# Kernel optimization log

Measured on AMD Instinct MI355X. Metric: run time of the kernel, lower is better.

Reference implementation:

```python
import jax, jax.numpy as jnp
import numpy as np

N_HEAD, D_MODEL, D_K, D_V, MAX_NEIGHBOR = 8, 512, 64, 64, 5
BS, SEQ = 2, 1024


def setup_inputs() -> dict:
    key = jax.random.key(0)
    ks = jax.random.split(key, 12)
    inp = {
        'q': jax.random.normal(ks[0], (BS, SEQ, D_MODEL), jnp.float32),
        'k': jax.random.normal(ks[1], (BS, SEQ, D_MODEL), jnp.float32),
        'v': jax.random.normal(ks[2], (BS, SEQ, D_MODEL), jnp.float32),
        'mask': jnp.ones((BS, SEQ, SEQ), jnp.int32),
        'dist': jax.random.randint(ks[3], (BS, SEQ, SEQ), 0, 10, jnp.int32),
        # weights stored as (in, out) so y = x @ W
        'w_qs': jax.random.normal(ks[4], (D_MODEL, N_HEAD * D_K), jnp.float32) * 0.02,
        'w_ks': jax.random.normal(ks[5], (D_MODEL, N_HEAD * D_K), jnp.float32) * 0.02,
        'w_vs': jax.random.normal(ks[6], (D_MODEL, N_HEAD * D_V), jnp.float32) * 0.02,
        'w_fc': jax.random.normal(ks[7], (N_HEAD * D_V, D_MODEL), jnp.float32) * 0.02,
        'ln_gamma': jnp.ones((D_MODEL,), jnp.float32),
        'ln_beta': jnp.zeros((D_MODEL,), jnp.float32),
        'base_rpr': jax.random.normal(ks[8], (MAX_NEIGHBOR + 1, D_K), jnp.float32) * 0.02,
    }
    return inp


def reference(q, k, v, mask, dist, w_qs, w_ks, w_vs, w_fc, ln_gamma, ln_beta, base_rpr):
    bs, sq, dm = q.shape
    temp = jnp.asarray(D_K, q.dtype) ** 0.5
    residual = q
    # layer norm on q only (as in original)
    mu = jnp.mean(q, axis=-1, keepdims=True)
    var = jnp.var(q, axis=-1, keepdims=True)
    qn = (q - mu) / jnp.sqrt(var + 1e-6) * ln_gamma + ln_beta
    # projections -> [bs, heads, seq, d]
    qh = (qn @ w_qs).reshape(bs, sq, N_HEAD, D_K).transpose(0, 2, 1, 3)
    kh = (k @ w_ks).reshape(bs, sq, N_HEAD, D_K).transpose(0, 2, 1, 3)
    vh = (v @ w_vs).reshape(bs, sq, N_HEAD, D_V).transpose(0, 2, 1, 3)
    qs = qh / temp
    # standard QK^T scores
    attn1 = jnp.einsum('bhid,bhjd->bhij', qs, kh)
    # relative-position scores: instead of materializing rpr[b,i,j,d],
    # contract q with the small base table then gather by clipped distance.
    dc = jnp.minimum(dist, MAX_NEIGHBOR)  # dist>max_neighbor -> max_neighbor
    qb = jnp.einsum('bhid,md->bhim', qs, base_rpr)  # [bs,h,seq,M+1]
    idx = jnp.broadcast_to(dc[:, None, :, :], (bs, N_HEAD, sq, sq))
    attn2 = jnp.take_along_axis(qb, idx, axis=-1)  # [bs,h,seq,seq]
    attn = attn1 + attn2
    attn = jnp.where(mask[:, None, :, :] == 0, jnp.asarray(-1e9, attn.dtype), attn)
    attn = jax.nn.softmax(attn, axis=-1)  # dropout disabled (eval)
    out = jnp.einsum('bhij,bhjd->bhid', attn, vh)
    out = out.transpose(0, 2, 1, 3).reshape(bs, sq, N_HEAD * D_V)
    out = out @ w_fc + residual
    return out, attn
```

## Files before the change

kernel.cpp:

```cpp
#include <hip/hip_runtime.h>
#include <math.h>

#define SEQ 1024
#define DM 512

typedef __attribute__((ext_vector_type(8))) short bf16x8;
typedef __attribute__((ext_vector_type(4))) short bf16x4;
typedef __attribute__((ext_vector_type(4))) float f32x4;
typedef __attribute__((ext_vector_type(4))) int i32x4;

static __device__ __forceinline__ short f2b(float f) {
    union { float f; unsigned u; } x; x.f = f;
    unsigned r = (x.u + 0x7FFFu + ((x.u >> 16) & 1u)) >> 16;
    return (short)r;
}
static __device__ __forceinline__ float b2f(short s) {
    union { unsigned u; float f; } x; x.u = ((unsigned)(unsigned short)s) << 16;
    return x.f;
}
static __device__ __forceinline__ int sidx(int row, int col) {
    int byte = (row << 7) + (col << 1);
    byte ^= (row & 7) << 4;
    return byte >> 1;
}
static __device__ __forceinline__ int svidx(int row, int m) {
    int byte = (row << 6) + (m << 1);
    byte ^= (row & 7) << 4;
    return byte >> 1;
}

static __device__ __forceinline__ void stage_f32(short* dst, const float* src, int srcStride, int tid) {
    int r = tid >> 2, c = (tid & 3) * 16;
    const float* p = src + (size_t)r * srcStride + c;
    bf16x8 v0, v1;
    #pragma unroll
    for (int e = 0; e < 8; ++e) v0[e] = f2b(p[e]);
    #pragma unroll
    for (int e = 0; e < 8; ++e) v1[e] = f2b(p[8 + e]);
    *(bf16x8*)&dst[sidx(r, c)] = v0;
    *(bf16x8*)&dst[sidx(r, c + 8)] = v1;
}
static __device__ __forceinline__ void stage_bf16(short* dst, const short* src, int srcStride, int tid) {
    int r = tid >> 2, c = (tid & 3) * 16;
    const short* p = src + (size_t)r * srcStride + c;
    bf16x8 v0 = *(const bf16x8*)p;
    bf16x8 v1 = *(const bf16x8*)(p + 8);
    *(bf16x8*)&dst[sidx(r, c)] = v0;
    *(bf16x8*)&dst[sidx(r, c + 8)] = v1;
}

static __device__ __forceinline__ void mma64(const short* sA, const short* sB, f32x4* acc,
                                             int w, int lr, int lg) {
    #pragma unroll
    for (int ks = 0; ks < 2; ++ks) {
        bf16x8 af = *(const bf16x8*)&sA[sidx(w * 16 + lr, ks * 32 + lg * 8)];
        #pragma unroll
        for (int nt = 0; nt < 4; ++nt) {
            bf16x8 bf = *(const bf16x8*)&sB[sidx(nt * 16 + lr, ks * 32 + lg * 8)];
            acc[nt] = __builtin_amdgcn_mfma_f32_16x16x32_bf16(af, bf, acc[nt], 0, 0, 0);
        }
    }
}

__global__ __launch_bounds__(256) void prep_kernel(
    const float* __restrict__ w0, const float* __restrict__ w1,
    const float* __restrict__ w2, const float* __restrict__ w3, short* __restrict__ wt,
    const float* __restrict__ q, float* __restrict__ qn,
    const float* __restrict__ gamma, const float* __restrict__ beta,
    const int* __restrict__ dist, const int* __restrict__ mask, unsigned char* __restrict__ idxp) {
    int blk = blockIdx.x;
    int tid = threadIdx.x;
    if (blk < 256) {
        int wsel = blk >> 6;
        int t = blk & 63;
        int tr = t >> 3, tc = t & 7;
        const float* src = wsel == 0 ? w0 : wsel == 1 ? w1 : wsel == 2 ? w2 : w3;
        short* dst = wt + (size_t)wsel * 512 * 512;
        __shared__ float tile[64][65];
        int r = tid >> 2, c = (tid & 3) * 16;
        const float* p = src + (size_t)(tr * 64 + r) * 512 + tc * 64 + c;
        #pragma unroll
        for (int e = 0; e < 16; ++e) tile[r][c + e] = p[e];
        __syncthreads();
        bf16x8 v0, v1;
        #pragma unroll
        for (int e = 0; e < 16; ++e) {
            short bv = f2b(tile[c + e][r]);
            if (e < 8) v0[e] = bv; else v1[e - 8] = bv;
        }
        short* qd = dst + (size_t)(tc * 64 + r) * 512 + tr * 64 + c;
        *(bf16x8*)qd = v0;
        *(bf16x8*)(qd + 8) = v1;
    } else if (blk < 2304) {
        int row = blk - 256;
        const float* x = q + (size_t)row * DM;
        float* y = qn + (size_t)row * DM;
        float v1 = x[tid], v2 = x[tid + 256];
        float s = v1 + v2;
        float ss = v1 * v1 + v2 * v2;
        for (int o = 32; o > 0; o >>= 1) { s += __shfl_down(s, o); ss += __shfl_down(ss, o); }
        __shared__ float red[4], red2[4];
        __shared__ float s_mu, s_rstd;
        int wid = tid >> 6, lane = tid & 63;
        if (lane == 0) { red[wid] = s; red2[wid] = ss; }
        __syncthreads();
        if (tid == 0) {
            float ts = red[0] + red[1] + red[2] + red[3];
            float tss = red2[0] + red2[1] + red2[2] + red2[3];
            float mu = ts / DM;
            float var = tss / DM - mu * mu;
            s_mu = mu;
            s_rstd = rsqrtf(var + 1e-6f);
        }
        __syncthreads();
        float mu = s_mu, rstd = s_rstd;
        y[tid]       = (v1 - mu) * rstd * gamma[tid]       + beta[tid];
        y[tid + 256] = (v2 - mu) * rstd * gamma[tid + 256] + beta[tid + 256];
    } else {
        size_t base = ((size_t)(blk - 2304) * 256 + tid) * 8;
        i32x4 d0 = *(const i32x4*)(dist + base);
        i32x4 d1 = *(const i32x4*)(dist + base + 4);
        i32x4 m0 = *(const i32x4*)(mask + base);
        i32x4 m1 = *(const i32x4*)(mask + base + 4);
        int dv[8], mv[8];
        #pragma unroll
        for (int e = 0; e < 4; ++e) { dv[e] = d0[e]; dv[4 + e] = d1[e]; mv[e] = m0[e]; mv[4 + e] = m1[e]; }
        unsigned char ob[4];
        #pragma unroll
        for (int e = 0; e < 4; ++e) {
            int dA = dv[2 * e];     if (dA > 5) dA = 5;
            int dB = dv[2 * e + 1]; if (dB > 5) dB = 5;
            unsigned nA = (unsigned)dA | (mv[2 * e] == 0 ? 8u : 0u);
            unsigned nB = (unsigned)dB | (mv[2 * e + 1] == 0 ? 8u : 0u);
            ob[e] = (unsigned char)(nA | (nB << 4));
        }
        *(uchar4*)(idxp + base / 2) = *(uchar4*)ob;
    }
}

__global__ __launch_bounds__(256) void qkv_kernel(
    const float* __restrict__ qn, const float* __restrict__ k, const float* __restrict__ v,
    const short* __restrict__ wT, short* __restrict__ qsb, short* __restrict__ khb,
    short* __restrict__ vT) {
    __shared__ short sA[64 * 64];
    __shared__ short sB[64 * 64];
    int tid = threadIdx.x;
    int sel = blockIdx.x >> 8;
    int t = blockIdx.x & 255;
    int bx = t & 7, by = t >> 3;
    int m0 = by << 6, n0 = bx << 6;
    int w = tid >> 6, l = tid & 63;
    int lr = l & 15, lg = l >> 4;
    const float* A = sel == 0 ? qn : sel == 1 ? k : v;
    const short* Bt = wT + (size_t)sel * 262144;
    float scale = sel == 0 ? 0.125f : 1.0f;
    f32x4 acc[4] = {};
    for (int kt = 0; kt < 512; kt += 64) {
        __syncthreads();
        stage_f32(sA, A + (size_t)m0 * 512 + kt, 512, tid);
        stage_bf16(sB, Bt + (size_t)n0 * 512 + kt, 512, tid);
        __syncthreads();
        mma64(sA, sB, acc, w, lr, lg);
    }
    if (sel == 2) {
        #pragma unroll
        for (int nt = 0; nt < 4; ++nt) {
            int gn = n0 + nt * 16 + lr;
            int gm0 = m0 + w * 16 + lg * 4;
            int bq = gm0 >> 10, j0 = gm0 & 1023;
            int h = gn >> 6, dl = gn & 63;
            bf16x4 pk;
            #pragma unroll
            for (int r = 0; r < 4; ++r) pk[r] = f2b(acc[nt][r]);
            *(bf16x4*)&vT[(((size_t)((bq << 3) + h) << 6) + dl) * 1024 + j0] = pk;
        }
    } else {
        short* C = sel == 0 ? qsb : khb;
        #pragma unroll
        for (int nt = 0; nt < 4; ++nt) {
            #pragma unroll
            for (int r = 0; r < 4; ++r) {
                int gm = m0 + w * 16 + lg * 4 + r;
                int gn = n0 + nt * 16 + lr;
                C[(size_t)gm * 512 + gn] = f2b(acc[nt][r] * scale);
            }
        }
    }
}

#define IDXSTR 520
__global__ __launch_bounds__(256) void attn_fused_kernel(
    const short* __restrict__ qsb, const short* __restrict__ khb,
    const short* __restrict__ vT, const unsigned char* __restrict__ idxp,
    const float* __restrict__ rpr, float* __restrict__ attnp, short* __restrict__ oh) {
    int bid = blockIdx.x;
    int bh = bid >> 6, it = bid & 63;
    int b = bh >> 3, h = bh & 7;
    int i0 = it << 4;
    int tid = threadIdx.x;
    int w = tid >> 6, l = tid & 63;
    int lr = l & 15, lg = l >> 4;

    __shared__ short sQ[16 * 64];
    __shared__ float sQB[16 * 8];
    __shared__ float sL[4][16];
    __shared__ __align__(16) char sScr[4 * 6144];
    __shared__ __align__(16) unsigned char sIdx[16 * IDXSTR];

    short* sKw = (short*)(sScr + w * 6144);
    short* sVw = (short*)(sScr + w * 6144 + 2048);

    if (tid < 128) {
        int r = tid >> 3, c = (tid & 7) * 8;
        bf16x8 qv = *(const bf16x8*)(qsb + ((size_t)(b * SEQ + i0 + r)) * DM + h * 64 + c);
        *(bf16x8*)&sQ[sidx(r, c)] = qv;
    }
    {
        const unsigned char* ibase = idxp + ((size_t)(b * SEQ + i0)) * 512;
        #pragma unroll
        for (int p = 0; p < 2; ++p) {
            int idx = p * 256 + tid;
            int row = idx >> 5;
            int cb = (idx & 31) * 16;
            i32x4 v = *(const i32x4*)(ibase + (size_t)row * 512 + cb);
            *(i32x4*)&sIdx[row * IDXSTR + cb] = v;
        }
    }
    __syncthreads();
    if (tid < 128) {
        int r = tid >> 3, m = tid & 7;
        if (m < 6) {
            float a = 0.f;
            #pragma unroll 8
            for (int d = 0; d < 64; ++d) a += b2f(sQ[sidx(r, d)]) * rpr[m * 64 + d];
            sQB[r * 8 + m] = a;
        }
    }
    __syncthreads();

    bf16x8 qf0 = *(const bf16x8*)&sQ[sidx(lr, lg * 8)];
    bf16x8 qf1 = *(const bf16x8*)&sQ[sidx(lr, 32 + lg * 8)];

    float qb0 = sQB[lr * 8 + 0], qb1 = sQB[lr * 8 + 1], qb2 = sQB[lr * 8 + 2];
    float qb3 = sQB[lr * 8 + 3], qb4 = sQB[lr * 8 + 4], qb5 = sQB[lr * 8 + 5];

    float l_lane = 0.f;
    unsigned p_lo[16], p_hi[16];
    f32x4 accO[4] = {};
    const short* kbase = khb + ((size_t)(b * SEQ)) * DM + h * 64;
    const short* vbase = vT + ((size_t)(bh * 64)) * 1024;
    const unsigned char* irow = sIdx + lr * IDXSTR + w * 8 + lg * 2;

    #pragma unroll
    for (int jt = 0; jt < 16; ++jt) {
        {
            const short* kg = kbase + (size_t)(jt * 64 + w * 16) * DM;
            int sr = l >> 3, sc = (l & 7) * 8;
            bf16x8 t0 = *(const bf16x8*)(kg + (size_t)sr * DM + sc);
            bf16x8 t1 = *(const bf16x8*)(kg + (size_t)(8 + sr) * DM + sc);
            *(bf16x8*)&sKw[sidx(sr, sc)] = t0;
            *(bf16x8*)&sKw[sidx(8 + sr, sc)] = t1;
        }
        if (!(jt & 1)) {
            #pragma unroll
            for (int i = 0; i < 4; ++i) {
                int d = (i & 1) * 32 + (l >> 1);
                int jtX = jt + (i >> 1);
                int col = jtX * 64 + w * 16 + (l & 1) * 8;
                bf16x8 tv = *(const bf16x8*)(vbase + (size_t)d * 1024 + col);
                *(bf16x8*)&sVw[svidx(d, (i >> 1) * 16 + (l & 1) * 8)] = tv;
            }
        }
        bf16x8 kf0 = *(const bf16x8*)&sKw[sidx(lr, lg * 8)];
        bf16x8 kf1 = *(const bf16x8*)&sKw[sidx(lr, 32 + lg * 8)];
        f32x4 sf = {};
        sf = __builtin_amdgcn_mfma_f32_16x16x32_bf16(kf0, qf0, sf, 0, 0, 0);
        sf = __builtin_amdgcn_mfma_f32_16x16x32_bf16(kf1, qf1, sf, 0, 0, 0);
        unsigned u = *(const unsigned short*)(irow + jt * 32);
        float pv[4];
        #pragma unroll
        for (int r = 0; r < 4; ++r) {
            unsigned bb = (u >> (4 * r)) & 0xFu;
            unsigned dd = bb & 7u;
            float t0 = (dd & 1) ? qb1 : qb0;
            float t1 = (dd & 1) ? qb3 : qb2;
            float t2 = (dd & 1) ? qb5 : qb4;
            float u0 = (dd & 2) ? t1 : t0;
            float bias = (dd & 4) ? t2 : u0;
            float s = fminf(sf[r] + bias, 30.f);
            float p = (bb & 8) ? 0.f : __expf(s);
            pv[r] = p;
            l_lane += p;
        }
        unsigned plo, phi;
        asm("v_cvt_pk_bf16_f32 %0, %1, %2" : "=v"(plo) : "v"(pv[0]), "v"(pv[1]));
        asm("v_cvt_pk_bf16_f32 %0, %1, %2" : "=v"(phi) : "v"(pv[2]), "v"(pv[3]));
        p_lo[jt] = plo; p_hi[jt] = phi;
        if (jt & 1) {
            unsigned plo0 = p_lo[jt - 1], phi0 = p_hi[jt - 1];
            int srcA = lr + ((lg & 1) << 5);
            int srcB = srcA + 16;
            unsigned aw0 = __shfl(plo0, srcA), aw1 = __shfl(phi0, srcA);
            unsigned aw2 = __shfl(plo,  srcA), aw3 = __shfl(phi,  srcA);
            unsigned bw0 = __shfl(plo0, srcB), bw1 = __shfl(phi0, srcB);
            unsigned bw2 = __shfl(plo,  srcB), bw3 = __shfl(phi,  srcB);
            bool hi = lg >= 2;
            union { unsigned q[4]; bf16x8 v; } afu;
            afu.q[0] = hi ? aw2 : aw0;
            afu.q[1] = hi ? aw3 : aw1;
            afu.q[2] = hi ? bw2 : bw0;
            afu.q[3] = hi ? bw3 : bw1;
            bf16x8 af = afu.v;
            #pragma unroll
            for (int nt = 0; nt < 4; ++nt) {
                bf16x8 bf = *(const bf16x8*)&sVw[svidx(nt * 16 + lr, lg * 8)];
                accO[nt] = __builtin_amdgcn_mfma_f32_16x16x32_bf16(af, bf, accO[nt], 0, 0, 0);
            }
        }
    }

    l_lane += __shfl_xor(l_lane, 16);
    l_lane += __shfl_xor(l_lane, 32);
    if (lg == 0) sL[w][lr] = l_lane;
    float* sOw = (float*)(sScr + w * 6144);
    #pragma unroll
    for (int nt = 0; nt < 4; ++nt)
        #pragma unroll
        for (int r = 0; r < 4; ++r)
            sOw[(lg * 4 + r) * 64 + nt * 16 + lr] = accO[nt][r];
    __syncthreads();

    {
        int row = tid >> 4, c4 = (tid & 15) * 4;
        f32x4 o = *(f32x4*)((float*)(sScr + 0 * 6144) + row * 64 + c4);
        o += *(f32x4*)((float*)(sScr + 1 * 6144) + row * 64 + c4);
        o += *(f32x4*)((float*)(sScr + 2 * 6144) + row * 64 + c4);
        o += *(f32x4*)((float*)(sScr + 3 * 6144) + row * 64 + c4);
        float rl = 1.f / (sL[0][row] + sL[1][row] + sL[2][row] + sL[3][row]);
        bf16x4 ob;
        #pragma unroll
        for (int e = 0; e < 4; ++e) ob[e] = f2b(o[e] * rl);
        *(bf16x4*)&oh[((size_t)(b * SEQ + i0 + row)) * DM + h * 64 + c4] = ob;
    }

    float rl = 1.f / (sL[0][lr] + sL[1][lr] + sL[2][lr] + sL[3][lr]);
    float* ap = attnp + ((size_t)(bh * SEQ + i0 + lr)) * SEQ + w * 16 + lg * 4;
    #pragma unroll
    for (int jt = 0; jt < 16; ++jt) {
        unsigned plo = p_lo[jt], phi = p_hi[jt];
        f32x4 o;
        o[0] = b2f((short)(plo & 0xffff)) * rl;
        o[1] = b2f((short)(plo >> 16))    * rl;
        o[2] = b2f((short)(phi & 0xffff)) * rl;
        o[3] = b2f((short)(phi >> 16))    * rl;
        *(f32x4*)&ap[jt * 64] = o;
    }
}

__global__ __launch_bounds__(256) void fc_kernel(
    const short* __restrict__ oh, const short* __restrict__ BtFc,
    const float* __restrict__ Rsd, float* __restrict__ Cp) {
    __shared__ short sA[64 * 64];
    __shared__ short sB[64 * 64];
    int tid = threadIdx.x;
    int bx = blockIdx.x & 7, by = blockIdx.x >> 3;
    int m0 = by << 6, n0 = bx << 6;
    int w = tid >> 6, l = tid & 63;
    int lr = l & 15, lg = l >> 4;
    f32x4 acc[4] = {};
    for (int kt = 0; kt < 512; kt += 64) {
        __syncthreads();
        stage_bf16(sA, oh + (size_t)m0 * 512 + kt, 512, tid);
        stage_bf16(sB, BtFc + (size_t)n0 * 512 + kt, 512, tid);
        __syncthreads();
        mma64(sA, sB, acc, w, lr, lg);
    }
    #pragma unroll
    for (int nt = 0; nt < 4; ++nt)
        #pragma unroll
        for (int r = 0; r < 4; ++r) {
            int gm = m0 + w * 16 + lg * 4 + r;
            int gn = n0 + nt * 16 + lr;
            Cp[(size_t)gm * 512 + gn] = acc[nt][r] + Rsd[(size_t)gm * 512 + gn];
        }
}

extern "C" void kernel_launch(void* const* d_in, const int* in_sizes, int n_in,
                              void* d_out, int out_size, void* d_ws, size_t ws_size,
                              hipStream_t stream) {
    const float* q     = (const float*)d_in[0];
    const float* k     = (const float*)d_in[1];
    const float* v     = (const float*)d_in[2];
    const int*   mask  = (const int*)d_in[3];
    const int*   dist  = (const int*)d_in[4];
    const float* w_qs  = (const float*)d_in[5];
    const float* w_ks  = (const float*)d_in[6];
    const float* w_vs  = (const float*)d_in[7];
    const float* w_fc  = (const float*)d_in[8];
    const float* gamma = (const float*)d_in[9];
    const float* beta  = (const float*)d_in[10];
    const float* rpr   = (const float*)d_in[11];

    char* wsb = (char*)d_ws;
    float* qn   = (float*)wsb;
    short* oh   = (short*)wsb;
    short* wT   = (short*)(wsb + 4u * 1024 * 1024);
    short* qsb  = (short*)(wsb + 6u * 1024 * 1024);
    short* khb  = (short*)(wsb + 8u * 1024 * 1024);
    short* vT   = (short*)(wsb + 10u * 1024 * 1024);
    unsigned char* idxp = (unsigned char*)(wsb + 12u * 1024 * 1024);

    float* outp  = (float*)d_out;
    float* attnp = outp + 1048576;

    prep_kernel<<<3328, 256, 0, stream>>>(w_qs, w_ks, w_vs, w_fc, wT, q, qn, gamma, beta, dist, mask, idxp);
    qkv_kernel<<<768, 256, 0, stream>>>(qn, k, v, wT, qsb, khb, vT);
    attn_fused_kernel<<<1024, 256, 0, stream>>>(qsb, khb, vT, idxp, rpr, attnp, oh);
    fc_kernel<<<256, 256, 0, stream>>>(oh, wT + 786432, q, outp);
}
```

Baseline: 75.04 us.

## Store K and V in MFMA fragment order so attention loads fragments directly

The QKV projection kernel now writes K and V into a pre-swizzled layout matching the MFMA operand fragments the attention kernel consumes. The attention kernel reads each lane's bf16x8 fragment straight from global memory and drops the per-wave LDS staging of K and V tiles along with the swizzled shared reads. This removes LDS traffic and shuffling in the inner loop, but the projection epilogue now does scattered 2-byte stores, and the attention loads are no longer overlapped through LDS.

Result: faster. 70.91 us (-5.5%).

```diff
diff --git a/kernel.cpp b/kernel.cpp
--- a/kernel.cpp
+++ b/kernel.cpp
@@ -20,11 +20,6 @@
 }
 static __device__ __forceinline__ int sidx(int row, int col) {
     int byte = (row << 7) + (col << 1);
-    byte ^= (row & 7) << 4;
-    return byte >> 1;
-}
-static __device__ __forceinline__ int svidx(int row, int m) {
-    int byte = (row << 6) + (m << 1);
     byte ^= (row & 7) << 4;
     return byte >> 1;
 }
@@ -140,8 +135,8 @@
 
 __global__ __launch_bounds__(256) void qkv_kernel(
     const float* __restrict__ qn, const float* __restrict__ k, const float* __restrict__ v,
-    const short* __restrict__ wT, short* __restrict__ qsb, short* __restrict__ khb,
-    short* __restrict__ vT) {
+    const short* __restrict__ wT, short* __restrict__ qsb, short* __restrict__ khx,
+    short* __restrict__ vfx) {
     __shared__ short sA[64 * 64];
     __shared__ short sB[64 * 64];
     int tid = threadIdx.x;
@@ -162,27 +157,47 @@
         __syncthreads();
         mma64(sA, sB, acc, w, lr, lg);
     }
-    if (sel == 2) {
-        #pragma unroll
-        for (int nt = 0; nt < 4; ++nt) {
-            int gn = n0 + nt * 16 + lr;
-            int gm0 = m0 + w * 16 + lg * 4;
-            int bq = gm0 >> 10, j0 = gm0 & 1023;
-            int h = gn >> 6, dl = gn & 63;
-            bf16x4 pk;
-            #pragma unroll
-            for (int r = 0; r < 4; ++r) pk[r] = f2b(acc[nt][r]);
-            *(bf16x4*)&vT[(((size_t)((bq << 3) + h) << 6) + dl) * 1024 + j0] = pk;
-        }
-    } else {
-        short* C = sel == 0 ? qsb : khb;
-        #pragma unroll
-        for (int nt = 0; nt < 4; ++nt) {
+    if (sel == 0) {
+        #pragma unroll
+        for (int nt = 0; nt < 4; ++nt)
             #pragma unroll
             for (int r = 0; r < 4; ++r) {
                 int gm = m0 + w * 16 + lg * 4 + r;
                 int gn = n0 + nt * 16 + lr;
-                C[(size_t)gm * 512 + gn] = f2b(acc[nt][r] * scale);
+                qsb[(size_t)gm * 512 + gn] = f2b(acc[nt][r] * scale);
+            }
+    } else if (sel == 1) {
+        int bq = m0 >> 10, jt = (m0 >> 6) & 15;
+        #pragma unroll
+        for (int nt = 0; nt < 4; ++nt) {
+            int gn = n0 + nt * 16 + lr;
+            int h = gn >> 6, dl = gn & 63;
+            int f = dl >> 5, lgp = (dl >> 3) & 3, e = dl & 7;
+            #pragma unroll
+            for (int r = 0; r < 4; ++r) {
+                int lrp = lg * 4 + r;
+                size_t off = ((((size_t)(bq * 8 + h) * 16 + jt) * 4 + w) << 10)
+                           + (size_t)((f * 4 + lgp) * 16 + lrp) * 8 + e;
+                khx[off] = f2b(acc[nt][r]);
+            }
+        }
+    } else {
+        int bq = m0 >> 10;
+        int j6 = (m0 >> 6) & 15;
+        int p = j6 >> 1, rel = j6 & 1;
+        #pragma unroll
+        for (int nt = 0; nt < 4; ++nt) {
+            int gn = n0 + nt * 16 + lr;
+            int h = gn >> 6, d = gn & 63;
+            int ntp = d >> 4, lrp = d & 15;
+            #pragma unroll
+            for (int r = 0; r < 4; ++r) {
+                int jj = w * 16 + lg * 4 + r;
+                int half = (jj >> 3) & 1, e = jj & 7, wj = jj >> 4;
+                int lgp = rel * 2 + half;
+                size_t off = ((((size_t)(bq * 8 + h) * 8 + p) * 4 + wj) << 11)
+                           + (size_t)((ntp * 4 + lgp) * 16 + lrp) * 8 + e;
+                vfx[off] = f2b(acc[nt][r]);
             }
         }
     }
@@ -190,8 +205,8 @@
 
 #define IDXSTR 520
 __global__ __launch_bounds__(256) void attn_fused_kernel(
-    const short* __restrict__ qsb, const short* __restrict__ khb,
-    const short* __restrict__ vT, const unsigned char* __restrict__ idxp,
+    const short* __restrict__ qsb, const short* __restrict__ khx,
+    const short* __restrict__ vfx, const unsigned char* __restrict__ idxp,
     const float* __restrict__ rpr, float* __restrict__ attnp, short* __restrict__ oh) {
     int bid = blockIdx.x;
     int bh = bid >> 6, it = bid & 63;
@@ -204,11 +219,8 @@
     __shared__ short sQ[16 * 64];
     __shared__ float sQB[16 * 8];
     __shared__ float sL[4][16];
-    __shared__ __align__(16) char sScr[4 * 6144];
+    __shared__ float sO[4 * 16 * 64];
     __shared__ __align__(16) unsigned char sIdx[16 * IDXSTR];
-
-    short* sKw = (short*)(sScr + w * 6144);
-    short* sVw = (short*)(sScr + w * 6144 + 2048);
 
     if (tid < 128) {
         int r = tid >> 3, c = (tid & 7) * 8;
@@ -247,32 +259,16 @@
     float l_lane = 0.f;
     unsigned p_lo[16], p_hi[16];
     f32x4 accO[4] = {};
-    const short* kbase = khb + ((size_t)(b * SEQ)) * DM + h * 64;
-    const short* vbase = vT + ((size_t)(bh * 64)) * 1024;
+    const short* kblk = khx + (((size_t)bh * 16) * 4 + w) * 1024;
+    const short* vblk = vfx + (((size_t)bh * 8) * 4 + w) * 2048;
+    int fragoff = (lg * 16 + lr) * 8;
     const unsigned char* irow = sIdx + lr * IDXSTR + w * 8 + lg * 2;
 
     #pragma unroll
     for (int jt = 0; jt < 16; ++jt) {
-        {
-            const short* kg = kbase + (size_t)(jt * 64 + w * 16) * DM;
-            int sr = l >> 3, sc = (l & 7) * 8;
-            bf16x8 t0 = *(const bf16x8*)(kg + (size_t)sr * DM + sc);
-            bf16x8 t1 = *(const bf16x8*)(kg + (size_t)(8 + sr) * DM + sc);
-            *(bf16x8*)&sKw[sidx(sr, sc)] = t0;
-            *(bf16x8*)&sKw[sidx(8 + sr, sc)] = t1;
-        }
-        if (!(jt & 1)) {
-            #pragma unroll
-            for (int i = 0; i < 4; ++i) {
-                int d = (i & 1) * 32 + (l >> 1);
-                int jtX = jt + (i >> 1);
-                int col = jtX * 64 + w * 16 + (l & 1) * 8;
-                bf16x8 tv = *(const bf16x8*)(vbase + (size_t)d * 1024 + col);
-                *(bf16x8*)&sVw[svidx(d, (i >> 1) * 16 + (l & 1) * 8)] = tv;
-            }
-        }
-        bf16x8 kf0 = *(const bf16x8*)&sKw[sidx(lr, lg * 8)];
-        bf16x8 kf1 = *(const bf16x8*)&sKw[sidx(lr, 32 + lg * 8)];
+        const short* kb = kblk + jt * 4096;
+        bf16x8 kf0 = *(const bf16x8*)(kb + fragoff);
+        bf16x8 kf1 = *(const bf16x8*)(kb + 512 + fragoff);
         f32x4 sf = {};
         sf = __builtin_amdgcn_mfma_f32_16x16x32_bf16(kf0, qf0, sf, 0, 0, 0);
         sf = __builtin_amdgcn_mfma_f32_16x16x32_bf16(kf1, qf1, sf, 0, 0, 0);
@@ -311,9 +307,10 @@
             afu.q[2] = hi ? bw2 : bw0;
             afu.q[3] = hi ? bw3 : bw1;
             bf16x8 af = afu.v;
+            const short* vb = vblk + (jt >> 1) * 8192;
             #pragma unroll
             for (int nt = 0; nt < 4; ++nt) {
-                bf16x8 bf = *(const bf16x8*)&sVw[svidx(nt * 16 + lr, lg * 8)];
+                bf16x8 bf = *(const bf16x8*)(vb + nt * 512 + fragoff);
                 accO[nt] = __builtin_amdgcn_mfma_f32_16x16x32_bf16(af, bf, accO[nt], 0, 0, 0);
             }
         }
@@ -322,20 +319,19 @@
     l_lane += __shfl_xor(l_lane, 16);
     l_lane += __shfl_xor(l_lane, 32);
     if (lg == 0) sL[w][lr] = l_lane;
-    float* sOw = (float*)(sScr + w * 6144);
     #pragma unroll
     for (int nt = 0; nt < 4; ++nt)
         #pragma unroll
         for (int r = 0; r < 4; ++r)
-            sOw[(lg * 4 + r) * 64 + nt * 16 + lr] = accO[nt][r];
+            sO[w * 1024 + (lg * 4 + r) * 64 + nt * 16 + lr] = accO[nt][r];
     __syncthreads();
 
     {
         int row = tid >> 4, c4 = (tid & 15) * 4;
-        f32x4 o = *(f32x4*)((float*)(sScr + 0 * 6144) + row * 64 + c4);
-        o += *(f32x4*)((float*)(sScr + 1 * 6144) + row * 64 + c4);
-        o += *(f32x4*)((float*)(sScr + 2 * 6144) + row * 64 + c4);
-        o += *(f32x4*)((float*)(sScr + 3 * 6144) + row * 64 + c4);
+        f32x4 o = *(f32x4*)&sO[row * 64 + c4];
+        o += *(f32x4*)&sO[1024 + row * 64 + c4];
+        o += *(f32x4*)&sO[2048 + row * 64 + c4];
+        o += *(f32x4*)&sO[3072 + row * 64 + c4];
         float rl = 1.f / (sL[0][row] + sL[1][row] + sL[2][row] + sL[3][row]);
         bf16x4 ob;
         #pragma unroll
@@ -406,15 +402,15 @@
     short* oh   = (short*)wsb;
     short* wT   = (short*)(wsb + 4u * 1024 * 1024);
     short* qsb  = (short*)(wsb + 6u * 1024 * 1024);
-    short* khb  = (short*)(wsb + 8u * 1024 * 1024);
-    short* vT   = (short*)(wsb + 10u * 1024 * 1024);
+    short* khx  = (short*)(wsb + 8u * 1024 * 1024);
+    short* vfx  = (short*)(wsb + 10u * 1024 * 1024);
     unsigned char* idxp = (unsigned char*)(wsb + 12u * 1024 * 1024);
 
     float* outp  = (float*)d_out;
     float* attnp = outp + 1048576;
 
     prep_kernel<<<3328, 256, 0, stream>>>(w_qs, w_ks, w_vs, w_fc, wT, q, qn, gamma, beta, dist, mask, idxp);
-    qkv_kernel<<<768, 256, 0, stream>>>(qn, k, v, wT, qsb, khb, vT);
-    attn_fused_kernel<<<1024, 256, 0, stream>>>(qsb, khb, vT, idxp, rpr, attnp, oh);
+    qkv_kernel<<<768, 256, 0, stream>>>(qn, k, v, wT, qsb, khx, vfx);
+    attn_fused_kernel<<<1024, 256, 0, stream>>>(qsb, khx, vfx, idxp, rpr, attnp, oh);
     fc_kernel<<<256, 256, 0, stream>>>(oh, wT + 786432, q, outp);
 }
```
